# Optimization experiments

Measured on AMD Instinct MI355X. Metric: run time of the kernel, lower is better.

Reference implementation:

```python
import jax, jax.numpy as jnp
import numpy as np

B, N, IN_DIM, HID, OUT_DIM = 8, 1024, 768, 128, 768
H1, H2, MHA_HEADS, C = 8, 1, 4, 32
ALPHA = 0.2
NEG = -9e15
LN_EPS = 1e-5


def _gat_layer(x, W, a1, a2, adj_mask):
    # x: [B,N,Fin], W: [H,Fin,Fout], a1/a2: [H,Fout], adj_mask: [B,N,N] bool
    h = jnp.einsum('bni,hio->bhno', x, W)                      # [B,H,N,F]
    s1 = jnp.einsum('bhno,ho->bhn', h, a1)                     # score for source node i
    s2 = jnp.einsum('bhno,ho->bhn', h, a2)                     # score for target node j
    e = jax.nn.leaky_relu(s1[:, :, :, None] + s2[:, :, None, :], negative_slope=ALPHA)
    e = jnp.where(adj_mask[:, None, :, :], e, NEG)
    attn = jax.nn.softmax(e, axis=-1)                          # [B,H,N,N]
    hp = jnp.einsum('bhnm,bhmo->bhno', attn, h)                # [B,H,N,F]
    b, nh, n, f = hp.shape
    return hp.transpose(0, 2, 1, 3).reshape(b, n, nh * f)      # concat heads -> [B,N,H*F]


def _mha(q, k, v, wq, bq, wk, bk, wv, bv, wo, bo, n_heads):
    # torch-style MultiheadAttention (eval, no dropout). q:[B,Lq,E] k,v:[B,Lk,E]
    b, lq, e = q.shape
    lk = k.shape[1]
    hd = e // n_heads
    Q = (q @ wq + bq).reshape(b, lq, n_heads, hd).transpose(0, 2, 1, 3)
    K = (k @ wk + bk).reshape(b, lk, n_heads, hd).transpose(0, 2, 1, 3)
    V = (v @ wv + bv).reshape(b, lk, n_heads, hd).transpose(0, 2, 1, 3)
    scores = jnp.einsum('bhqd,bhkd->bhqk', Q, K) / jnp.sqrt(jnp.float32(hd))
    attn = jax.nn.softmax(scores, axis=-1)
    out = jnp.einsum('bhqk,bhkd->bhqd', attn, V)
    out = out.transpose(0, 2, 1, 3).reshape(b, lq, e)
    return out @ wo + bo


def _layernorm(x, g, b):
    mu = jnp.mean(x, axis=-1, keepdims=True)
    var = jnp.var(x, axis=-1, keepdims=True)
    return (x - mu) * jax.lax.rsqrt(var + LN_EPS) * g + b


def setup_inputs() -> dict:
    key = jax.random.key(0)
    ks = jax.random.split(key, 24)
    s = lambda fan_in: 1.0 / np.sqrt(fan_in)
    inp = {
        'node_features': jax.random.normal(ks[0], (B, N, IN_DIM), jnp.float32),
        'adjacency': jax.random.randint(ks[1], (B, N, N), 0, 2, jnp.int32),
        'context_indices': jax.random.randint(ks[2], (B, C), 0, N, jnp.int32),
        # GAT layer 1: 8 heads, in=768 -> out=128 each
        'W1': jax.random.normal(ks[3], (H1, IN_DIM, HID), jnp.float32) * s(IN_DIM),
        'a1_1': jax.random.normal(ks[4], (H1, HID), jnp.float32) * s(2 * HID),
        'a2_1': jax.random.normal(ks[5], (H1, HID), jnp.float32) * s(2 * HID),
        # GAT layer 2: 1 head, in=1024 -> out=128
        'W2': jax.random.normal(ks[6], (H2, HID * H1, HID), jnp.float32) * s(HID * H1),
        'a1_2': jax.random.normal(ks[7], (H2, HID), jnp.float32) * s(2 * HID),
        'a2_2': jax.random.normal(ks[8], (H2, HID), jnp.float32) * s(2 * HID),
        # query MultiheadAttention (embed_dim=128, 4 heads)
        'wq': jax.random.normal(ks[9], (HID, HID), jnp.float32) * s(HID),
        'bq': jnp.zeros((HID,), jnp.float32),
        'wk': jax.random.normal(ks[10], (HID, HID), jnp.float32) * s(HID),
        'bk': jnp.zeros((HID,), jnp.float32),
        'wv': jax.random.normal(ks[11], (HID, HID), jnp.float32) * s(HID),
        'bv': jnp.zeros((HID,), jnp.float32),
        'wo': jax.random.normal(ks[12], (HID, HID), jnp.float32) * s(HID),
        'bo': jnp.zeros((HID,), jnp.float32),
        # projection MLP
        'p1_w': jax.random.normal(ks[13], (HID, HID), jnp.float32) * s(HID),
        'p1_b': jnp.zeros((HID,), jnp.float32),
        'ln_g': jnp.ones((HID,), jnp.float32),
        'ln_b': jnp.zeros((HID,), jnp.float32),
        'p2_w': jax.random.normal(ks[14], (HID, OUT_DIM), jnp.float32) * s(HID),
        'p2_b': jnp.zeros((OUT_DIM,), jnp.float32),
    }
    return inp


def reference(node_features, adjacency, context_indices,
              W1, a1_1, a2_1, W2, a1_2, a2_2,
              wq, bq, wk, bk, wv, bv, wo, bo,
              p1_w, p1_b, ln_g, ln_b, p2_w, p2_b):
    adj_mask = adjacency > 0
    h = jax.nn.elu(_gat_layer(node_features, W1, a1_1, a2_1, adj_mask))  # [B,N,1024]
    h = jax.nn.elu(_gat_layer(h, W2, a1_2, a2_2, adj_mask))              # [B,N,128]
    q = h[:, 0:1, :]                                                      # [B,1,E]
    ctx = jnp.take_along_axis(h, context_indices[:, :, None], axis=1)     # [B,C,E]
    pooled = _mha(q, ctx, ctx, wq, bq, wk, bk, wv, bv, wo, bo, MHA_HEADS)[:, 0, :]
    z = jax.nn.relu(_layernorm(pooled @ p1_w + p1_b, ln_g, ln_b))
    return z @ p2_w + p2_b                                                # [B,OUT_DIM]
```

## Files before the change

kernel.cpp:

```cpp
#include <hip/hip_runtime.h>
#include <hip/hip_bf16.h>

#define ALPHA 0.2f
#define LOG2E 1.4426950408889634f

using short8  = __attribute__((ext_vector_type(8))) short;
using short4v = __attribute__((ext_vector_type(4))) short;
using f32x4   = __attribute__((ext_vector_type(4))) float;
using int4v   = __attribute__((ext_vector_type(4))) int;

static __device__ __forceinline__ float b2f(short s) {
    union { float f; unsigned u; } v; v.u = ((unsigned)(unsigned short)s) << 16; return v.f;
}
static __device__ __forceinline__ short f2bf(float f) {
    __hip_bfloat16 h = __float2bfloat16(f);
    return *reinterpret_cast<short*>(&h);
}
static __device__ __forceinline__ float fexp2(float x) {
    return __builtin_amdgcn_exp2f(x);
}
static __device__ __forceinline__ void gload_lds16(const void* g, void* l) {
    __builtin_amdgcn_global_load_lds(
        (const __attribute__((address_space(1))) unsigned*)g,
        (__attribute__((address_space(3))) unsigned*)l, 16, 0, 0);
}

__global__ __launch_bounds__(256) void k_prep(
        const int* __restrict__ adj, unsigned* __restrict__ adjb,
        const float* __restrict__ x, short* __restrict__ xb,
        const float* __restrict__ W1, short* __restrict__ W1T,
        const float* __restrict__ W2, short* __restrict__ W2T) {
    int bid = blockIdx.x, t = threadIdx.x;
    if (bid < 32768) {
        int idx = bid * 256 + t;
        int lane = t & 63;
        unsigned long long m = __ballot(adj[idx] > 0);
        if ((lane & 31) == 0) adjb[idx >> 5] = (unsigned)(m >> (lane & 32));
    } else if (bid < 38912) {
        int idx = (bid - 32768) * 256 + t;
        f32x4 v = ((const f32x4*)x)[idx];
        short4v o;
        o[0] = f2bf(v[0]); o[1] = f2bf(v[1]); o[2] = f2bf(v[2]); o[3] = f2bf(v[3]);
        ((short4v*)xb)[idx] = o;
    } else if (bid < 41984) {
        int idx = (bid - 38912) * 256 + t;
        int n = idx / 768, k = idx - n * 768;
        int h = n >> 7, o = n & 127;
        W1T[idx] = f2bf(W1[(h * 768 + k) * 128 + o]);
    } else {
        int idx = (bid - 41984) * 256 + t;
        int n = idx >> 10, k = idx & 1023;
        W2T[idx] = f2bf(W2[k * 128 + n]);
    }
}

__global__ __launch_bounds__(256) void k_gemm_bt(
        const short* __restrict__ A, const short* __restrict__ Bt,
        short* __restrict__ Ct, int K, int Ncols) {
    int tid = threadIdx.x, wave = tid >> 6, lane = tid & 63;
    int lr = lane & 15, lg = lane >> 4;
    int flat = blockIdx.y * gridDim.x + blockIdx.x;
    int chunkw = (gridDim.x * gridDim.y) >> 3;
    int swz = (flat & 7) * chunkw + (flat >> 3);
    int bx = swz % gridDim.x, by = swz / gridDim.x;
    int m0 = bx * 128, n0 = by * 128;
    int wm = (wave >> 1) * 64, wn = (wave & 1) * 64;
    __shared__ short lsA[2][128 * 64], lsB[2][128 * 64];
    f32x4 acc[4][4];
#pragma unroll
    for (int i = 0; i < 4; i++)
#pragma unroll
        for (int j = 0; j < 4; j++) acc[i][j] = (f32x4){0.f, 0.f, 0.f, 0.f};

    auto stage = [&](int bufsel, int k0) {
#pragma unroll
        for (int s = 0; s < 4; s++) {
            int chunk = s * 256 + tid;
            int r = chunk >> 3, c = chunk & 7;
            int csrc = c ^ (r & 7);
            gload_lds16(A + (size_t)(m0 + r) * K + k0 + csrc * 8, &lsA[bufsel][chunk * 8]);
            gload_lds16(Bt + (size_t)(n0 + r) * K + k0 + csrc * 8, &lsB[bufsel][chunk * 8]);
        }
    };
    auto compute = [&](const short* la, const short* lb) {
#pragma unroll
        for (int kk = 0; kk < 2; kk++) {
            short8 a[4], bb[4];
#pragma unroll
            for (int f = 0; f < 4; f++) {
                int ra = wm + f * 16 + lr, rb = wn + f * 16 + lr;
                a[f]  = *(const short8*)(la + ra * 64 + (((kk * 4 + lg) ^ (ra & 7)) * 8));
                bb[f] = *(const short8*)(lb + rb * 64 + (((kk * 4 + lg) ^ (rb & 7)) * 8));
            }
#pragma unroll
            for (int fm = 0; fm < 4; fm++)
#pragma unroll
                for (int fn = 0; fn < 4; fn++)
                    acc[fm][fn] = __builtin_amdgcn_mfma_f32_16x16x32_bf16(a[fm], bb[fn], acc[fm][fn], 0, 0, 0);
        }
    };
    stage(0, 0);
    __syncthreads();
    for (int k2 = 0; k2 < K; k2 += 128) {
        stage(1, k2 + 64);
        compute(lsA[0], lsB[0]);
        __syncthreads();
        if (k2 + 128 < K) stage(0, k2 + 128);
        compute(lsA[1], lsB[1]);
        __syncthreads();
    }
#pragma unroll
    for (int fm = 0; fm < 4; fm++) {
        int mb = m0 + wm + fm * 16 + lg * 4;
        size_t obase = ((size_t)(mb >> 10) * Ncols) * 1024 + (mb & 1023);
#pragma unroll
        for (int fn = 0; fn < 4; fn++) {
            int n = n0 + wn + fn * 16 + lr;
            short4v st;
            st[0] = f2bf(acc[fm][fn][0]); st[1] = f2bf(acc[fm][fn][1]);
            st[2] = f2bf(acc[fm][fn][2]); st[3] = f2bf(acc[fm][fn][3]);
            *(short4v*)(Ct + obase + (size_t)n * 1024) = st;
        }
    }
}

__global__ __launch_bounds__(256) void k_gemm64(
        const short* __restrict__ A, const short* __restrict__ Bt,
        short* __restrict__ Ct, int K, int Ncols) {
    int tid = threadIdx.x, wave = tid >> 6, lane = tid & 63;
    int lr = lane & 15, lg = lane >> 4;
    int flat = blockIdx.y * gridDim.x + blockIdx.x;
    int chunkw = (gridDim.x * gridDim.y) >> 3;
    int swz = (flat & 7) * chunkw + (flat >> 3);
    int bx = swz % gridDim.x, by = swz / gridDim.x;
    int m0 = bx * 64, n0 = by * 64;
    int wm = (wave >> 1) * 32, wn = (wave & 1) * 32;
    __shared__ short lsA[2][64 * 32], lsB[2][64 * 32];
    f32x4 acc[2][2];
#pragma unroll
    for (int i = 0; i < 2; i++)
#pragma unroll
        for (int j = 0; j < 2; j++) acc[i][j] = (f32x4){0.f, 0.f, 0.f, 0.f};

    auto stage = [&](int bufsel, int k0) {
        int r = tid >> 2, c = tid & 3;
        int csrc = c ^ (r & 3);
        int base = (wave * 64) * 8;
        gload_lds16(A + (size_t)(m0 + r) * K + k0 + csrc * 8, &lsA[bufsel][base]);
        gload_lds16(Bt + (size_t)(n0 + r) * K + k0 + csrc * 8, &lsB[bufsel][base]);
    };
    stage(0, 0);
    __syncthreads();
    int buf = 0;
    for (int k0 = 0; k0 < K; k0 += 32) {
        if (k0 + 32 < K) stage(buf ^ 1, k0 + 32);
        short8 a[2], bb[2];
#pragma unroll
        for (int f = 0; f < 2; f++) {
            int ra = wm + f * 16 + lr, rb = wn + f * 16 + lr;
            a[f]  = *(const short8*)(&lsA[buf][ra * 32 + ((lg ^ (ra & 3)) * 8)]);
            bb[f] = *(const short8*)(&lsB[buf][rb * 32 + ((lg ^ (rb & 3)) * 8)]);
        }
#pragma unroll
        for (int fm = 0; fm < 2; fm++)
#pragma unroll
            for (int fn = 0; fn < 2; fn++)
                acc[fm][fn] = __builtin_amdgcn_mfma_f32_16x16x32_bf16(a[fm], bb[fn], acc[fm][fn], 0, 0, 0);
        __syncthreads();
        buf ^= 1;
    }
#pragma unroll
    for (int fm = 0; fm < 2; fm++) {
        int mb = m0 + wm + fm * 16 + lg * 4;
        size_t obase = ((size_t)(mb >> 10) * Ncols) * 1024 + (mb & 1023);
#pragma unroll
        for (int fn = 0; fn < 2; fn++) {
            int n = n0 + wn + fn * 16 + lr;
            short4v st;
            st[0] = f2bf(acc[fm][fn][0]); st[1] = f2bf(acc[fm][fn][1]);
            st[2] = f2bf(acc[fm][fn][2]); st[3] = f2bf(acc[fm][fn][3]);
            *(short4v*)(Ct + obase + (size_t)n * 1024) = st;
        }
    }
}

__global__ __launch_bounds__(256) void k_s12(
        const short* __restrict__ ht, const float* __restrict__ a1,
        const float* __restrict__ a2, float* __restrict__ s1,
        float* __restrict__ s2, int nh) {
    int bh = blockIdx.x;
    int h = bh % nh;
    int i4 = threadIdx.x * 4;
    const short* base = ht + (size_t)bh * 131072 + i4;
    f32x4 acc1 = {0.f, 0.f, 0.f, 0.f}, acc2 = {0.f, 0.f, 0.f, 0.f};
#pragma unroll 8
    for (int o = 0; o < 128; o++) {
        short4v v = *(const short4v*)(base + ((size_t)o << 10));
        float w1 = a1[h * 128 + o], w2 = a2[h * 128 + o];
#pragma unroll
        for (int r = 0; r < 4; r++) {
            float f = b2f(v[r]);
            acc1[r] += f * w1;
            acc2[r] += f * w2;
        }
    }
#pragma unroll
    for (int r = 0; r < 4; r++) { acc1[r] *= LOG2E; acc2[r] *= LOG2E; }
    *(f32x4*)(s1 + bh * 1024 + i4) = acc1;
    *(f32x4*)(s2 + bh * 1024 + i4) = acc2;
}

__global__ __launch_bounds__(512) void k_attn1(
        const short* __restrict__ ht, const unsigned* __restrict__ adjb,
        const float* __restrict__ s1, const float* __restrict__ s2,
        short* __restrict__ out) {
    int flat = blockIdx.y * 8 + blockIdx.x;
    int swz = (flat & 7) * 64 + (flat >> 3);
    int bh = swz >> 3, bxi = swz & 7;
    int b = bh >> 3, h = bh & 7;
    int tid = threadIdx.x, wave = tid >> 6, lane = tid & 63;
    int lr = lane & 15, lg = lane >> 4;
    int ic = bxi * 128 + wave * 16 + lr;
    int row = bh * 1024 + ic;
    float s1i = s1[row];
    const unsigned long long* abrow =
        (const unsigned long long*)(adjb + ((size_t)(b << 10) + ic) * 32);
    const float* s2r = s2 + bh * 1024;
    const short* hbase = ht + (size_t)bh * 131072;

    __shared__ short lsh[2][16384];
    f32x4 acc[8];
#pragma unroll
    for (int f = 0; f < 8; f++) acc[f] = (f32x4){0.f, 0.f, 0.f, 0.f};
    float psum = 0.f;

    auto stage = [&](int bufsel, int j0) {
#pragma unroll
        for (int s = 0; s < 4; s++) {
            int chunk = s * 512 + tid;
            int r = chunk >> 4, c = chunk & 15;
            int csrc = c ^ (r & 15);
            gload_lds16(hbase + (size_t)r * 1024 + j0 + csrc * 8,
                        &lsh[bufsel][chunk * 8]);
        }
    };
    auto compute = [&](const short* ls, int j0) {
        unsigned long long aw0 = abrow[j0 >> 6], aw1 = abrow[(j0 >> 6) + 1];
#pragma unroll
        for (int kk = 0; kk < 4; kk++) {
            int jb = j0 + kk * 32 + lg * 8;
            f32x4 t0 = *(const f32x4*)(s2r + jb);
            f32x4 t1 = *(const f32x4*)(s2r + jb + 4);
            unsigned long long aw = (kk < 2) ? aw0 : aw1;
            unsigned bits = (unsigned)(aw >> ((kk & 1) * 32 + lg * 8)) & 0xFFu;
            float pv[8];
#pragma unroll
            for (int e = 0; e < 8; e++) {
                float sv = e < 4 ? t0[e] : t1[e & 3];
                float ee = s1i + sv;
                ee = fmaxf(ee, ALPHA * ee);
                float p = fexp2(ee);
                p = ((bits >> e) & 1) ? p : 0.f;
                pv[e] = p;
                psum += p;
            }
            int4v pw;
#pragma unroll
            for (int w = 0; w < 4; w++) {
                int d;
                asm("v_cvt_pk_bf16_f32 %0, %1, %2"
                    : "=v"(d) : "v"(pv[2 * w]), "v"(pv[2 * w + 1]));
                pw[w] = d;
            }
            short8 pb = __builtin_bit_cast(short8, pw);
#pragma unroll
            for (int fm = 0; fm < 8; fm++) {
                int r = fm * 16 + lr;
                int ck = (kk * 4 + lg) ^ (r & 15);
                short8 af = *(const short8*)(ls + r * 128 + ck * 8);
                acc[fm] = __builtin_amdgcn_mfma_f32_16x16x32_bf16(af, pb, acc[fm], 0, 0, 0);
            }
        }
    };

    stage(0, 0);
    __syncthreads();
    for (int t2 = 0; t2 < 1024; t2 += 256) {
        stage(1, t2 + 128);
        compute(lsh[0], t2);
        __syncthreads();
        if (t2 + 256 < 1024) stage(0, t2 + 256);
        compute(lsh[1], t2 + 128);
        __syncthreads();
    }
    psum += __shfl_xor(psum, 16);
    psum += __shfl_xor(psum, 32);
    float rdi = 1.f / psum;
    size_t orow = ((size_t)(b << 10) + ic) * 1024 + h * 128;
#pragma unroll
    for (int fm = 0; fm < 8; fm++) {
        int ob = (fm << 4) + lg * 4;
        short4v st;
#pragma unroll
        for (int r = 0; r < 4; r++) {
            float x = acc[fm][r] * rdi;
            x = x > 0.f ? x : expm1f(x);
            st[r] = f2bf(x);
        }
        *(short4v*)(out + orow + ob) = st;
    }
}

__global__ __launch_bounds__(256) void k_attn2g(
        const short* __restrict__ h2t, const unsigned* __restrict__ adjb,
        const float* __restrict__ s1, const float* __restrict__ s2,
        const int* __restrict__ cidx, float* __restrict__ ghat) {
    int tile = blockIdx.x;
    int b = blockIdx.y;
    int tid = threadIdx.x, wave = tid >> 6, lane = tid & 63;
    int lr = lane & 15, lg = lane >> 4;

    __shared__ int nodes[16];
    __shared__ float sps[4][16];
    __shared__ float sacc[4][16][129];

    if (tid < 16) {
        int pos = tile * 16 + tid;
        int nd = 0;
        if (pos >= 1 && pos <= 32) nd = cidx[b * 32 + pos - 1];
        nodes[tid] = nd;
    }
    __syncthreads();

    const float* s2r = s2 + b * 1024;
    int nd = nodes[lr];
    float s1i = s1[b * 1024 + nd];
    const unsigned long long* abrow =
        (const unsigned long long*)(adjb + ((size_t)(b << 10) + nd) * 32);
    const short* hb = h2t + (size_t)b * 131072;
    f32x4 acc[8];
#pragma unroll
    for (int f = 0; f < 8; f++) acc[f] = (f32x4){0.f, 0.f, 0.f, 0.f};
    float psum = 0.f;

    for (int j0 = wave * 256; j0 < wave * 256 + 256; j0 += 32) {
        int jb = j0 + lg * 8;
        f32x4 t0 = *(const f32x4*)(s2r + jb);
        f32x4 t1 = *(const f32x4*)(s2r + jb + 4);
        unsigned bits = (unsigned)(abrow[j0 >> 6] >> ((j0 & 32) + lg * 8)) & 0xFFu;
        short8 pb;
#pragma unroll
        for (int e = 0; e < 8; e++) {
            float sv = e < 4 ? t0[e] : t1[e & 3];
            float ee = s1i + sv;
            ee = fmaxf(ee, ALPHA * ee);
            float p = fexp2(ee);
            p = ((bits >> e) & 1) ? p : 0.f;
            psum += p;
            pb[e] = f2bf(p);
        }
#pragma unroll
        for (int fm = 0; fm < 8; fm++) {
            short8 af = *(const short8*)(hb + (size_t)(fm * 16 + lr) * 1024 + jb);
            acc[fm] = __builtin_amdgcn_mfma_f32_16x16x32_bf16(af, pb, acc[fm], 0, 0, 0);
        }
    }
    psum += __shfl_xor(psum, 16);
    psum += __shfl_xor(psum, 32);
    if (lg == 0) sps[wave][lr] = psum;
#pragma unroll
    for (int fm = 0; fm < 8; fm++)
#pragma unroll
        for (int r = 0; r < 4; r++)
            sacc[wave][lr][fm * 16 + lg * 4 + r] = acc[fm][r];
    __syncthreads();
    for (int e = tid; e < 2048; e += 256) {
        int li = e >> 7, o = e & 127;
        float sum = sps[0][li] + sps[1][li] + sps[2][li] + sps[3][li];
        float v = (sacc[0][li][o] + sacc[1][li][o] + sacc[2][li][o] + sacc[3][li][o]) / sum;
        v = v > 0.f ? v : expm1f(v);
        ghat[((size_t)b * 48 + tile * 16 + li) * 128 + o] = v;
    }
}

__global__ __launch_bounds__(256) void k_qkv(
        const float* __restrict__ ghat,
        const float* __restrict__ wk, const float* __restrict__ bk,
        const float* __restrict__ wvp, const float* __restrict__ bv,
        float* __restrict__ Kp, float* __restrict__ Vp) {
    int b = blockIdx.y, rg = blockIdx.x & 7, o0 = (blockIdx.x >> 3) * 64;
    int t = threadIdx.x, wvi = t >> 6, ln = t & 63;
    __shared__ float sx[4][128];
    __shared__ float sWk[128 * 64], sWv[128 * 64];

    if (wvi < 2) {
        int cb = wvi * 64;
        gload_lds16(ghat + ((size_t)b * 48 + 1 + rg * 4) * 128 + (size_t)(cb + ln) * 4,
                    (float*)sx + cb * 4);
    }
#pragma unroll
    for (int s = 0; s < 8; s++) {
        int cb = s * 256 + wvi * 64;
        int q = cb + ln, rw = q >> 4, c4 = q & 15;
        gload_lds16(wk  + (size_t)rw * 128 + o0 + c4 * 4, &sWk[cb * 4]);
        gload_lds16(wvp + (size_t)rw * 128 + o0 + c4 * 4, &sWv[cb * 4]);
    }
    __syncthreads();
    int o = o0 + ln;
    float ka = bk[o], va = bv[o];
#pragma unroll 32
    for (int c = 0; c < 128; c++) {
        float x = sx[wvi][c];
        ka += x * sWk[c * 64 + ln];
        va += x * sWv[c * 64 + ln];
    }
    int r = rg * 4 + wvi;
    Kp[((size_t)b * 32 + r) * 128 + o] = ka;
    Vp[((size_t)b * 32 + r) * 128 + o] = va;
}

__global__ __launch_bounds__(256) void k_tail(
        const float* __restrict__ ghat, const float* __restrict__ Kp,
        const float* __restrict__ Vp,
        const float* __restrict__ wq, const float* __restrict__ bq,
        const float* __restrict__ wo, const float* __restrict__ bo,
        const float* __restrict__ p1w, const float* __restrict__ p1b,
        const float* __restrict__ lng, const float* __restrict__ lnb,
        float* __restrict__ tvec) {
    int b = blockIdx.x, t = threadIdx.x;
    int wvi = t >> 6, ln = t & 63;
    __shared__ float sq[128], sQ[128], sK[32][128], sV[32][128];
    __shared__ float sP[4][33], sO[128], sT[128], sZ[128];
    __shared__ float sred[2];
    __shared__ float sW[128 * 128];

#pragma unroll
    for (int s = 0; s < 4; s++) {
        int cb = s * 256 + wvi * 64;
        gload_lds16(Kp + (size_t)b * 4096 + (size_t)(cb + ln) * 4, (float*)sK + cb * 4);
        gload_lds16(Vp + (size_t)b * 4096 + (size_t)(cb + ln) * 4, (float*)sV + cb * 4);
    }
#pragma unroll
    for (int s = 0; s < 16; s++) {
        int cb = s * 256 + wvi * 64;
        gload_lds16(wq + (size_t)(cb + ln) * 4, &sW[cb * 4]);
    }
    if (t < 128) sq[t] = ghat[(size_t)b * 48 * 128 + t];
    __syncthreads();
    if (t < 128) {
        float a0 = 0.f, a1 = 0.f, a2 = 0.f, a3 = 0.f;
#pragma unroll
        for (int c = 0; c < 128; c += 4) {
            a0 += sq[c]     * sW[c * 128 + t];
            a1 += sq[c + 1] * sW[(c + 1) * 128 + t];
            a2 += sq[c + 2] * sW[(c + 2) * 128 + t];
            a3 += sq[c + 3] * sW[(c + 3) * 128 + t];
        }
        sQ[t] = bq[t] + ((a0 + a1) + (a2 + a3));
    }
    __syncthreads();
#pragma unroll
    for (int s = 0; s < 16; s++) {
        int cb = s * 256 + wvi * 64;
        gload_lds16(wo + (size_t)(cb + ln) * 4, &sW[cb * 4]);
    }
    if (t < 128) {
        int hh = t >> 5, jj = t & 31;
        float s = 0.f;
#pragma unroll
        for (int d = 0; d < 32; d++) s += sQ[hh * 32 + d] * sK[jj][hh * 32 + d];
        s *= 0.17677669529663687f;
        float m = s;
#pragma unroll
        for (int off = 16; off > 0; off >>= 1) m = fmaxf(m, __shfl_xor(m, off, 32));
        float p = __expf(s - m);
        float sum = p;
#pragma unroll
        for (int off = 16; off > 0; off >>= 1) sum += __shfl_xor(sum, off, 32);
        sP[hh][jj] = p / sum;
    }
    __syncthreads();
    if (t < 128) {
        int hh = t >> 5;
        float s = 0.f;
#pragma unroll
        for (int jj = 0; jj < 32; jj++) s += sP[hh][jj] * sV[jj][t];
        sO[t] = s;
    }
    __syncthreads();
    if (t < 128) {
        float a0 = 0.f, a1 = 0.f, a2 = 0.f, a3 = 0.f;
#pragma unroll
        for (int c = 0; c < 128; c += 4) {
            a0 += sO[c]     * sW[c * 128 + t];
            a1 += sO[c + 1] * sW[(c + 1) * 128 + t];
            a2 += sO[c + 2] * sW[(c + 2) * 128 + t];
            a3 += sO[c + 3] * sW[(c + 3) * 128 + t];
        }
        sT[t] = bo[t] + ((a0 + a1) + (a2 + a3));
    }
    __syncthreads();
#pragma unroll
    for (int s = 0; s < 16; s++) {
        int cb = s * 256 + wvi * 64;
        gload_lds16(p1w + (size_t)(cb + ln) * 4, &sW[cb * 4]);
    }
    __syncthreads();
    if (t < 128) {
        float a0 = 0.f, a1 = 0.f, a2 = 0.f, a3 = 0.f;
#pragma unroll
        for (int c = 0; c < 128; c += 4) {
            a0 += sT[c]     * sW[c * 128 + t];
            a1 += sT[c + 1] * sW[(c + 1) * 128 + t];
            a2 += sT[c + 2] * sW[(c + 2) * 128 + t];
            a3 += sT[c + 3] * sW[(c + 3) * 128 + t];
        }
        sZ[t] = p1b[t] + ((a0 + a1) + (a2 + a3));
    }
    __syncthreads();
    if (t < 64) {
        float v = sZ[t] + sZ[t + 64];
#pragma unroll
        for (int off = 32; off > 0; off >>= 1) v += __shfl_xor(v, off);
        if (t == 0) sred[0] = v * (1.f / 128.f);
    }
    __syncthreads();
    float mu = sred[0];
    if (t < 64) {
        float d1 = sZ[t] - mu, d2 = sZ[t + 64] - mu;
        float v = d1 * d1 + d2 * d2;
#pragma unroll
        for (int off = 32; off > 0; off >>= 1) v += __shfl_xor(v, off);
        if (t == 0) sred[1] = v * (1.f / 128.f);
    }
    __syncthreads();
    float rstd = rsqrtf(sred[1] + 1e-5f);
    if (t < 128) {
        float z = (sZ[t] - mu) * rstd * lng[t] + lnb[t];
        tvec[b * 128 + t] = fmaxf(z, 0.f);
    }
}

__global__ __launch_bounds__(256) void k_p2(
        const float* __restrict__ tvec, const float* __restrict__ p2w,
        const float* __restrict__ p2b, float* __restrict__ out) {
    int jj0 = blockIdx.x * 128, b = blockIdx.y;
    int t = threadIdx.x, wvi = t >> 6, ln = t & 63;
    __shared__ float sT[128];
    __shared__ float sW[128 * 128];

#pragma unroll
    for (int s = 0; s < 16; s++) {
        int cb = s * 256 + wvi * 64;
        int q = cb + ln, c = q >> 5, c4 = q & 31;
        gload_lds16(p2w + (size_t)c * 768 + jj0 + c4 * 4, &sW[cb * 4]);
    }
    if (t < 128) sT[t] = tvec[b * 128 + t];
    __syncthreads();
    if (t < 128) {
        float a0 = 0.f, a1 = 0.f, a2 = 0.f, a3 = 0.f;
#pragma unroll
        for (int c = 0; c < 128; c += 4) {
            a0 += sT[c]     * sW[c * 128 + t];
            a1 += sT[c + 1] * sW[(c + 1) * 128 + t];
            a2 += sT[c + 2] * sW[(c + 2) * 128 + t];
            a3 += sT[c + 3] * sW[(c + 3) * 128 + t];
        }
        out[b * 768 + jj0 + t] = p2b[jj0 + t] + ((a0 + a1) + (a2 + a3));
    }
}

extern "C" void kernel_launch(void* const* d_in, const int* in_sizes, int n_in,
                              void* d_out, int out_size, void* d_ws, size_t ws_size,
                              hipStream_t stream) {
    const float* x   = (const float*)d_in[0];
    const int*  adj  = (const int*)d_in[1];
    const int*  cidx = (const int*)d_in[2];
    const float* W1  = (const float*)d_in[3];
    const float* a11 = (const float*)d_in[4];
    const float* a21 = (const float*)d_in[5];
    const float* W2  = (const float*)d_in[6];
    const float* a12 = (const float*)d_in[7];
    const float* a22 = (const float*)d_in[8];
    const float* wq = (const float*)d_in[9];  const float* bq = (const float*)d_in[10];
    const float* wk = (const float*)d_in[11]; const float* bk = (const float*)d_in[12];
    const float* wv = (const float*)d_in[13]; const float* bv = (const float*)d_in[14];
    const float* wo = (const float*)d_in[15]; const float* bo = (const float*)d_in[16];
    const float* p1w = (const float*)d_in[17]; const float* p1b = (const float*)d_in[18];
    const float* lng = (const float*)d_in[19]; const float* lnb = (const float*)d_in[20];
    const float* p2w = (const float*)d_in[21]; const float* p2b = (const float*)d_in[22];
    float* out = (float*)d_out;

    char* ws = (char*)d_ws;
    size_t off = 0;
    auto alloc = [&](size_t bytes) -> char* {
        char* p = ws + off;
        off = (off + bytes + 255) & ~(size_t)255;
        return p;
    };
    short* Xb   = (short*)alloc(8192ull * 768 * 2);
    short* W1T  = (short*)alloc(1024ull * 768 * 2);
    short* W2T  = (short*)alloc(128ull * 1024 * 2);
    unsigned* adjb = (unsigned*)alloc(8ull * 1024 * 32 * 4);
    short* h1t  = (short*)alloc(64ull * 128 * 1024 * 2);
    float* s1a  = (float*)alloc(64ull * 1024 * 4);
    float* s2a  = (float*)alloc(64ull * 1024 * 4);
    short* hcat = (short*)alloc(8192ull * 1024 * 2);
    short* h2t  = (short*)alloc(8ull * 128 * 1024 * 2);
    float* s1b  = (float*)alloc(8192ull * 4);
    float* s2b  = (float*)alloc(8192ull * 4);
    float* ghat = (float*)alloc(8ull * 48 * 128 * 4);
    float* Kp   = (float*)alloc(8ull * 32 * 128 * 4);
    float* Vp   = (float*)alloc(8ull * 32 * 128 * 4);
    float* tvec = (float*)alloc(8ull * 128 * 4);
    if (off > ws_size) return;

    k_prep<<<42496, 256, 0, stream>>>(adj, adjb, x, Xb, W1, W1T, W2, W2T);

    k_gemm_bt<<<dim3(64, 8), 256, 0, stream>>>(Xb, W1T, h1t, 768, 1024);
    k_s12<<<64, 256, 0, stream>>>(h1t, a11, a21, s1a, s2a, 8);
    k_attn1<<<dim3(8, 64), 512, 0, stream>>>(h1t, adjb, s1a, s2a, hcat);

    k_gemm64<<<dim3(128, 2), 256, 0, stream>>>(hcat, W2T, h2t, 1024, 128);
    k_s12<<<8, 256, 0, stream>>>(h2t, a12, a22, s1b, s2b, 1);
    k_attn2g<<<dim3(3, 8), 256, 0, stream>>>(h2t, adjb, s1b, s2b, cidx, ghat);

    k_qkv<<<dim3(16, 8), 256, 0, stream>>>(ghat, wk, bk, wv, bv, Kp, Vp);
    k_tail<<<8, 256, 0, stream>>>(ghat, Kp, Vp, wq, bq, wo, bo,
                                  p1w, p1b, lng, lnb, tvec);
    k_p2<<<dim3(6, 8), 256, 0, stream>>>(tvec, p2w, p2b, out);
}
```

Before: 161.0 us.

## Fuse GAT score projection into GEMM epilogue; give attn1 waves two row tiles

The first GEMM epilogue now computes the per-head s1/s2 attention score dot products directly from fp32 accumulators, using shuffle and LDS reductions, so the separate k_s12 launch for layer 1 disappears. k_attn1 drops to 256 threads where each wave handles two 16-row tiles, so every LDS B-fragment load feeds two MFMAs and the staging work per block is split over fewer threads. The scores are now taken from fp32 accumulators rather than bf16-rounded h, which changes numerics slightly. The doubled accumulators raise register pressure and may lower occupancy.

After: 177.6 us. 1.1x slower.

```diff
diff --git a/kernel.cpp b/kernel.cpp
--- a/kernel.cpp
+++ b/kernel.cpp
@@ -56,7 +56,9 @@
 
 __global__ __launch_bounds__(256) void k_gemm_bt(
         const short* __restrict__ A, const short* __restrict__ Bt,
-        short* __restrict__ Ct, int K, int Ncols) {
+        short* __restrict__ Ct, int K, int Ncols,
+        const float* __restrict__ a1, const float* __restrict__ a2,
+        float* __restrict__ s1, float* __restrict__ s2) {
     int tid = threadIdx.x, wave = tid >> 6, lane = tid & 63;
     int lr = lane & 15, lg = lane >> 4;
     int flat = blockIdx.y * gridDim.x + blockIdx.x;
@@ -66,6 +68,7 @@
     int m0 = bx * 128, n0 = by * 128;
     int wm = (wave >> 1) * 64, wn = (wave & 1) * 64;
     __shared__ short lsA[2][128 * 64], lsB[2][128 * 64];
+    __shared__ float sred1[2][128], sred2[2][128];
     f32x4 acc[4][4];
 #pragma unroll
     for (int i = 0; i < 4; i++)
@@ -120,6 +123,43 @@
             st[0] = f2bf(acc[fm][fn][0]); st[1] = f2bf(acc[fm][fn][1]);
             st[2] = f2bf(acc[fm][fn][2]); st[3] = f2bf(acc[fm][fn][3]);
             *(short4v*)(Ct + obase + (size_t)n * 1024) = st;
+        }
+    }
+    if (a1 != nullptr) {
+        int h = by;
+        float av1[4], av2[4];
+#pragma unroll
+        for (int fn = 0; fn < 4; fn++) {
+            int o = wn + fn * 16 + lr;
+            av1[fn] = a1[h * 128 + o];
+            av2[fn] = a2[h * 128 + o];
+        }
+        int wcol = wave & 1;
+#pragma unroll
+        for (int fm = 0; fm < 4; fm++)
+#pragma unroll
+            for (int r = 0; r < 4; r++) {
+                float v1 = acc[fm][0][r] * av1[0] + acc[fm][1][r] * av1[1]
+                         + acc[fm][2][r] * av1[2] + acc[fm][3][r] * av1[3];
+                float v2 = acc[fm][0][r] * av2[0] + acc[fm][1][r] * av2[1]
+                         + acc[fm][2][r] * av2[2] + acc[fm][3][r] * av2[3];
+#pragma unroll
+                for (int off = 1; off < 16; off <<= 1) {
+                    v1 += __shfl_xor(v1, off);
+                    v2 += __shfl_xor(v2, off);
+                }
+                if (lr == 0) {
+                    int il = wm + fm * 16 + lg * 4 + r;
+                    sred1[wcol][il] = v1;
+                    sred2[wcol][il] = v2;
+                }
+            }
+        __syncthreads();
+        if (tid < 128) {
+            int b = m0 >> 10;
+            int irow = (b * 8 + h) * 1024 + (m0 & 1023) + tid;
+            s1[irow] = (sred1[0][tid] + sred1[1][tid]) * LOG2E;
+            s2[irow] = (sred2[0][tid] + sred2[1][tid]) * LOG2E;
         }
     }
 }
@@ -210,7 +250,7 @@
     *(f32x4*)(s2 + bh * 1024 + i4) = acc2;
 }
 
-__global__ __launch_bounds__(512) void k_attn1(
+__global__ __launch_bounds__(256) void k_attn1(
         const short* __restrict__ ht, const unsigned* __restrict__ adjb,
         const float* __restrict__ s1, const float* __restrict__ s2,
         short* __restrict__ out) {
@@ -220,24 +260,30 @@
     int b = bh >> 3, h = bh & 7;
     int tid = threadIdx.x, wave = tid >> 6, lane = tid & 63;
     int lr = lane & 15, lg = lane >> 4;
-    int ic = bxi * 128 + wave * 16 + lr;
-    int row = bh * 1024 + ic;
-    float s1i = s1[row];
-    const unsigned long long* abrow =
-        (const unsigned long long*)(adjb + ((size_t)(b << 10) + ic) * 32);
+    int ic0 = bxi * 128 + wave * 32 + lr;
+    int ic1 = ic0 + 16;
+    float s1i0 = s1[bh * 1024 + ic0];
+    float s1i1 = s1[bh * 1024 + ic1];
+    const unsigned long long* ab0 =
+        (const unsigned long long*)(adjb + ((size_t)(b << 10) + ic0) * 32);
+    const unsigned long long* ab1 =
+        (const unsigned long long*)(adjb + ((size_t)(b << 10) + ic1) * 32);
     const float* s2r = s2 + bh * 1024;
     const short* hbase = ht + (size_t)bh * 131072;
 
     __shared__ short lsh[2][16384];
-    f32x4 acc[8];
-#pragma unroll
-    for (int f = 0; f < 8; f++) acc[f] = (f32x4){0.f, 0.f, 0.f, 0.f};
-    float psum = 0.f;
+    f32x4 acc[8][2];
+#pragma unroll
+    for (int f = 0; f < 8; f++) {
+        acc[f][0] = (f32x4){0.f, 0.f, 0.f, 0.f};
+        acc[f][1] = (f32x4){0.f, 0.f, 0.f, 0.f};
+    }
+    float psum0 = 0.f, psum1 = 0.f;
 
     auto stage = [&](int bufsel, int j0) {
 #pragma unroll
-        for (int s = 0; s < 4; s++) {
-            int chunk = s * 512 + tid;
+        for (int s = 0; s < 8; s++) {
+            int chunk = s * 256 + tid;
             int r = chunk >> 4, c = chunk & 15;
             int csrc = c ^ (r & 15);
             gload_lds16(hbase + (size_t)r * 1024 + j0 + csrc * 8,
@@ -245,40 +291,48 @@
         }
     };
     auto compute = [&](const short* ls, int j0) {
-        unsigned long long aw0 = abrow[j0 >> 6], aw1 = abrow[(j0 >> 6) + 1];
+        unsigned long long a00 = ab0[j0 >> 6], a01 = ab0[(j0 >> 6) + 1];
+        unsigned long long a10 = ab1[j0 >> 6], a11 = ab1[(j0 >> 6) + 1];
 #pragma unroll
         for (int kk = 0; kk < 4; kk++) {
             int jb = j0 + kk * 32 + lg * 8;
             f32x4 t0 = *(const f32x4*)(s2r + jb);
             f32x4 t1 = *(const f32x4*)(s2r + jb + 4);
-            unsigned long long aw = (kk < 2) ? aw0 : aw1;
-            unsigned bits = (unsigned)(aw >> ((kk & 1) * 32 + lg * 8)) & 0xFFu;
-            float pv[8];
+            int sh = (kk & 1) * 32 + lg * 8;
+            unsigned bits0 = (unsigned)(((kk < 2) ? a00 : a01) >> sh) & 0xFFu;
+            unsigned bits1 = (unsigned)(((kk < 2) ? a10 : a11) >> sh) & 0xFFu;
+            float pv0[8], pv1[8];
 #pragma unroll
             for (int e = 0; e < 8; e++) {
                 float sv = e < 4 ? t0[e] : t1[e & 3];
-                float ee = s1i + sv;
-                ee = fmaxf(ee, ALPHA * ee);
-                float p = fexp2(ee);
-                p = ((bits >> e) & 1) ? p : 0.f;
-                pv[e] = p;
-                psum += p;
+                float e0 = s1i0 + sv, e1 = s1i1 + sv;
+                e0 = fmaxf(e0, ALPHA * e0);
+                e1 = fmaxf(e1, ALPHA * e1);
+                float p0 = fexp2(e0), p1 = fexp2(e1);
+                p0 = ((bits0 >> e) & 1) ? p0 : 0.f;
+                p1 = ((bits1 >> e) & 1) ? p1 : 0.f;
+                pv0[e] = p0; pv1[e] = p1;
+                psum0 += p0; psum1 += p1;
             }
-            int4v pw;
+            int4v pw0, pw1;
 #pragma unroll
             for (int w = 0; w < 4; w++) {
-                int d;
+                int d0, d1;
                 asm("v_cvt_pk_bf16_f32 %0, %1, %2"
-                    : "=v"(d) : "v"(pv[2 * w]), "v"(pv[2 * w + 1]));
-                pw[w] = d;
+                    : "=v"(d0) : "v"(pv0[2 * w]), "v"(pv0[2 * w + 1]));
+                asm("v_cvt_pk_bf16_f32 %0, %1, %2"
+                    : "=v"(d1) : "v"(pv1[2 * w]), "v"(pv1[2 * w + 1]));
+                pw0[w] = d0; pw1[w] = d1;
             }
-            short8 pb = __builtin_bit_cast(short8, pw);
+            short8 pb0 = __builtin_bit_cast(short8, pw0);
+            short8 pb1 = __builtin_bit_cast(short8, pw1);
 #pragma unroll
             for (int fm = 0; fm < 8; fm++) {
                 int r = fm * 16 + lr;
                 int ck = (kk * 4 + lg) ^ (r & 15);
                 short8 af = *(const short8*)(ls + r * 128 + ck * 8);
-                acc[fm] = __builtin_amdgcn_mfma_f32_16x16x32_bf16(af, pb, acc[fm], 0, 0, 0);
+                acc[fm][0] = __builtin_amdgcn_mfma_f32_16x16x32_bf16(af, pb0, acc[fm][0], 0, 0, 0);
+                acc[fm][1] = __builtin_amdgcn_mfma_f32_16x16x32_bf16(af, pb1, acc[fm][1], 0, 0, 0);
             }
         }
     };
@@ -293,21 +347,28 @@
         compute(lsh[1], t2 + 128);
         __syncthreads();
     }
-    psum += __shfl_xor(psum, 16);
-    psum += __shfl_xor(psum, 32);
-    float rdi = 1.f / psum;
-    size_t orow = ((size_t)(b << 10) + ic) * 1024 + h * 128;
+    psum0 += __shfl_xor(psum0, 16);
+    psum0 += __shfl_xor(psum0, 32);
+    psum1 += __shfl_xor(psum1, 16);
+    psum1 += __shfl_xor(psum1, 32);
+    float rdi0 = 1.f / psum0, rdi1 = 1.f / psum1;
+    size_t orow0 = ((size_t)(b << 10) + ic0) * 1024 + h * 128;
+    size_t orow1 = ((size_t)(b << 10) + ic1) * 1024 + h * 128;
 #pragma unroll
     for (int fm = 0; fm < 8; fm++) {
         int ob = (fm << 4) + lg * 4;
-        short4v st;
+        short4v st0, st1;
 #pragma unroll
         for (int r = 0; r < 4; r++) {
-            float x = acc[fm][r] * rdi;
-            x = x > 0.f ? x : expm1f(x);
-            st[r] = f2bf(x);
-        }
-        *(short4v*)(out + orow + ob) = st;
+            float x0 = acc[fm][0][r] * rdi0;
+            float x1 = acc[fm][1][r] * rdi1;
+            x0 = x0 > 0.f ? x0 : expm1f(x0);
+            x1 = x1 > 0.f ? x1 : expm1f(x1);
+            st0[r] = f2bf(x0);
+            st1[r] = f2bf(x1);
+        }
+        *(short4v*)(out + orow0 + ob) = st0;
+        *(short4v*)(out + orow1 + ob) = st1;
     }
 }
 
@@ -617,9 +678,9 @@
 
     k_prep<<<42496, 256, 0, stream>>>(adj, adjb, x, Xb, W1, W1T, W2, W2T);
 
-    k_gemm_bt<<<dim3(64, 8), 256, 0, stream>>>(Xb, W1T, h1t, 768, 1024);
-    k_s12<<<64, 256, 0, stream>>>(h1t, a11, a21, s1a, s2a, 8);
-    k_attn1<<<dim3(8, 64), 512, 0, stream>>>(h1t, adjb, s1a, s2a, hcat);
+    k_gemm_bt<<<dim3(64, 8), 256, 0, stream>>>(Xb, W1T, h1t, 768, 1024,
+                                               a11, a21, s1a, s2a);
+    k_attn1<<<dim3(8, 64), 256, 0, stream>>>(h1t, adjb, s1a, s2a, hcat);
 
     k_gemm64<<<dim3(128, 2), 256, 0, stream>>>(hcat, W2T, h2t, 1024, 128);
     k_s12<<<8, 256, 0, stream>>>(h2t, a12, a22, s1b, s2b, 1);
```

## Fuse GAT score projections into GEMM epilogue and compute softmax denominator via MFMA

Applied to the files above, without the earlier changes.

The layer-1 GEMM epilogue now computes the s1/s2 attention score dot products from the fp32 accumulators, using shuffle and LDS reductions, so the separate k_s12 launch and its re-read of h1t are gone. In the attention kernel, the per-lane row-sum of probabilities is replaced by an extra MFMA against a ones vector, removing the scalar adds and the cross-lane shuffles. Scores now come from fp32 accumulators rather than from rounded bf16 values, which slightly changes numerics. The row sum now accumulates bf16-rounded probabilities, so the denominator matches the weights actually used.

Result: faster. 155.6 us (-3.3%).

```diff
diff --git a/kernel.cpp b/kernel.cpp
--- a/kernel.cpp
+++ b/kernel.cpp
@@ -56,7 +56,9 @@
 
 __global__ __launch_bounds__(256) void k_gemm_bt(
         const short* __restrict__ A, const short* __restrict__ Bt,
-        short* __restrict__ Ct, int K, int Ncols) {
+        short* __restrict__ Ct, int K, int Ncols,
+        const float* __restrict__ a1, const float* __restrict__ a2,
+        float* __restrict__ s1, float* __restrict__ s2) {
     int tid = threadIdx.x, wave = tid >> 6, lane = tid & 63;
     int lr = lane & 15, lg = lane >> 4;
     int flat = blockIdx.y * gridDim.x + blockIdx.x;
@@ -66,6 +68,7 @@
     int m0 = bx * 128, n0 = by * 128;
     int wm = (wave >> 1) * 64, wn = (wave & 1) * 64;
     __shared__ short lsA[2][128 * 64], lsB[2][128 * 64];
+    __shared__ float sred1[2][128], sred2[2][128];
     f32x4 acc[4][4];
 #pragma unroll
     for (int i = 0; i < 4; i++)
@@ -120,6 +123,43 @@
             st[0] = f2bf(acc[fm][fn][0]); st[1] = f2bf(acc[fm][fn][1]);
             st[2] = f2bf(acc[fm][fn][2]); st[3] = f2bf(acc[fm][fn][3]);
             *(short4v*)(Ct + obase + (size_t)n * 1024) = st;
+        }
+    }
+    if (a1 != nullptr) {
+        int h = by;
+        float av1[4], av2[4];
+#pragma unroll
+        for (int fn = 0; fn < 4; fn++) {
+            int o = wn + fn * 16 + lr;
+            av1[fn] = a1[h * 128 + o];
+            av2[fn] = a2[h * 128 + o];
+        }
+        int wcol = wave & 1;
+#pragma unroll
+        for (int fm = 0; fm < 4; fm++)
+#pragma unroll
+            for (int r = 0; r < 4; r++) {
+                float v1 = acc[fm][0][r] * av1[0] + acc[fm][1][r] * av1[1]
+                         + acc[fm][2][r] * av1[2] + acc[fm][3][r] * av1[3];
+                float v2 = acc[fm][0][r] * av2[0] + acc[fm][1][r] * av2[1]
+                         + acc[fm][2][r] * av2[2] + acc[fm][3][r] * av2[3];
+#pragma unroll
+                for (int off = 1; off < 16; off <<= 1) {
+                    v1 += __shfl_xor(v1, off);
+                    v2 += __shfl_xor(v2, off);
+                }
+                if (lr == 0) {
+                    int il = wm + fm * 16 + lg * 4 + r;
+                    sred1[wcol][il] = v1;
+                    sred2[wcol][il] = v2;
+                }
+            }
+        __syncthreads();
+        if (tid < 128) {
+            int b = m0 >> 10;
+            int irow = (b * 8 + h) * 1024 + (m0 & 1023) + tid;
+            s1[irow] = (sred1[0][tid] + sred1[1][tid]) * LOG2E;
+            s2[irow] = (sred2[0][tid] + sred2[1][tid]) * LOG2E;
         }
     }
 }
@@ -232,7 +272,10 @@
     f32x4 acc[8];
 #pragma unroll
     for (int f = 0; f < 8; f++) acc[f] = (f32x4){0.f, 0.f, 0.f, 0.f};
-    float psum = 0.f;
+    f32x4 accs = (f32x4){0.f, 0.f, 0.f, 0.f};
+    short8 ones8;
+#pragma unroll
+    for (int e = 0; e < 8; e++) ones8[e] = (short)0x3F80;
 
     auto stage = [&](int bufsel, int j0) {
 #pragma unroll
@@ -260,9 +303,7 @@
                 float ee = s1i + sv;
                 ee = fmaxf(ee, ALPHA * ee);
                 float p = fexp2(ee);
-                p = ((bits >> e) & 1) ? p : 0.f;
-                pv[e] = p;
-                psum += p;
+                pv[e] = ((bits >> e) & 1) ? p : 0.f;
             }
             int4v pw;
 #pragma unroll
@@ -273,6 +314,7 @@
                 pw[w] = d;
             }
             short8 pb = __builtin_bit_cast(short8, pw);
+            accs = __builtin_amdgcn_mfma_f32_16x16x32_bf16(ones8, pb, accs, 0, 0, 0);
 #pragma unroll
             for (int fm = 0; fm < 8; fm++) {
                 int r = fm * 16 + lr;
@@ -293,9 +335,7 @@
         compute(lsh[1], t2 + 128);
         __syncthreads();
     }
-    psum += __shfl_xor(psum, 16);
-    psum += __shfl_xor(psum, 32);
-    float rdi = 1.f / psum;
+    float rdi = 1.f / accs[0];
     size_t orow = ((size_t)(b << 10) + ic) * 1024 + h * 128;
 #pragma unroll
     for (int fm = 0; fm < 8; fm++) {
@@ -617,8 +657,8 @@
 
     k_prep<<<42496, 256, 0, stream>>>(adj, adjb, x, Xb, W1, W1T, W2, W2T);
 
-    k_gemm_bt<<<dim3(64, 8), 256, 0, stream>>>(Xb, W1T, h1t, 768, 1024);
-    k_s12<<<64, 256, 0, stream>>>(h1t, a11, a21, s1a, s2a, 8);
+    k_gemm_bt<<<dim3(64, 8), 256, 0, stream>>>(Xb, W1T, h1t, 768, 1024,
+                                               a11, a21, s1a, s2a);
     k_attn1<<<dim3(8, 64), 512, 0, stream>>>(h1t, adjb, s1a, s2a, hcat);
 
     k_gemm64<<<dim3(128, 2), 256, 0, stream>>>(hcat, W2T, h2t, 1024, 128);
```
